# Kernel optimization log

Hardware: AMD Instinct MI355X
Metric: run time of the kernel (lower is better)

Reference implementation:

```python
import jax, jax.numpy as jnp
import numpy as np

UNITS = 1024
IN_DIM = 1024
BATCH = 64
SEQ = 512


def setup_inputs() -> dict:
    key = jax.random.key(0)
    k_x, k_wf, k_wb = jax.random.split(key, 3)
    x = jax.random.normal(k_x, (BATCH, SEQ, IN_DIM), dtype=jnp.float32)
    # keras 'random_normal' initializer -> stddev 0.05
    W_fwd = jax.random.normal(k_wf, (IN_DIM + UNITS, 4 * UNITS), dtype=jnp.float32) * 0.05
    b_fwd = jnp.zeros((4 * UNITS,), dtype=jnp.float32)
    W_bwd = jax.random.normal(k_wb, (IN_DIM + UNITS, 4 * UNITS), dtype=jnp.float32) * 0.05
    b_bwd = jnp.zeros((4 * UNITS,), dtype=jnp.float32)
    return {"x": x, "W_fwd": W_fwd, "b_fwd": b_fwd, "W_bwd": W_bwd, "b_bwd": b_bwd}


def _lstm_scan(x_tbd, W, b, units, reverse):
    # x_tbd: [T, B, D] time-major
    B = x_tbd.shape[1]
    h0 = jnp.zeros((B, units), dtype=x_tbd.dtype)
    c0 = jnp.zeros((B, units), dtype=x_tbd.dtype)

    def step(carry, x_t):
        h, c = carry
        z = jnp.concatenate([x_t, h], axis=-1) @ W + b  # [B, 4U]
        zi, zf, zo, zg = jnp.split(z, 4, axis=-1)
        c_new = jax.nn.sigmoid(zf) * c + jax.nn.sigmoid(zi) * jnp.tanh(zg)
        h_new = jax.nn.sigmoid(zo) * jnp.tanh(c_new)
        return (h_new, c_new), h_new

    _, hs = jax.lax.scan(step, (h0, c0), x_tbd, reverse=reverse)
    return hs  # [T, B, U], aligned with input time order


def reference(x, W_fwd, b_fwd, W_bwd, b_bwd):
    x_tbd = jnp.transpose(x, (1, 0, 2))  # [T, B, D]
    h_fwd = _lstm_scan(x_tbd, W_fwd, b_fwd, UNITS, reverse=False)
    h_bwd = _lstm_scan(x_tbd, W_bwd, b_bwd, UNITS, reverse=True)
    h = jnp.concatenate([h_fwd, h_bwd], axis=-1)  # [T, B, 2U]
    return jnp.transpose(h, (1, 0, 2))  # [B, T, 2U]
```

## Files before the change

kernel.cpp:

```cpp
#include <hip/hip_runtime.h>
#include <stdint.h>

#define B_ 64
#define T_ 512
#define D_ 1024
#define U_ 1024
#define G4_ 4096
#define M_ (B_ * T_)
#define ZLD 65

typedef unsigned short u16;
typedef float f32x4 __attribute__((ext_vector_type(4)));
typedef _Float16 f16x8 __attribute__((ext_vector_type(8)));
typedef unsigned short u16x4 __attribute__((ext_vector_type(4)));

__device__ __forceinline__ u16 f2h(float f) {
  union { _Float16 h; u16 u; } v; v.h = (_Float16)f; return v.u;
}
__device__ __forceinline__ float h2f(uint32_t u) {
  union { _Float16 h; u16 u; } v; v.u = (u16)u; return (float)v.h;
}
__device__ __forceinline__ float sigm(float x) { return 1.f / (1.f + __expf(-x)); }
__device__ __forceinline__ float tanhf_(float x) {
  x = fminf(12.f, fmaxf(-12.f, x));
  float e = __expf(2.f * x);
  return (e - 1.f) / (e + 1.f);
}

__device__ __forceinline__ void glds16(const void* g, void* l) {
  __builtin_amdgcn_global_load_lds(
      (const __attribute__((address_space(1))) uint32_t*)g,
      (__attribute__((address_space(3))) uint32_t*)l, 16, 0, 0);
}

template <int R>
__device__ __forceinline__ void stage_tile(const char* gbase, long gs, char* lds, int tid) {
  const int lane = tid & 63, wid = tid >> 6;
#pragma unroll
  for (int j = wid; j < R / 8; j += 4) {
    const int row = j * 8 + (lane >> 3);
    const int lg = ((lane & 7) * 16) ^ ((row & 7) << 4);
    glds16(gbase + (long)row * gs + lg, lds + j * 1024);
  }
}

__device__ __forceinline__ f16x8 read_frag(const char* lds, int row, int kbyte) {
  const int ph = row * 128 + (kbyte ^ ((row & 7) << 4));
  return *(const f16x8*)(lds + ph);
}

#define MFMA_(a, b, c) __builtin_amdgcn_mfma_f32_16x16x32_f16(a, b, c, 0, 0, 0)
#define BAR_LGKM() asm volatile("s_waitcnt lgkmcnt(0)\n\ts_barrier" ::: "memory")


__global__ __launch_bounds__(256) void cast_x_kernel(const float* __restrict__ x,
                                                     u16* __restrict__ xb) {
  const long n = (long)M_ * D_ / 4;
  for (long i = (long)blockIdx.x * blockDim.x + threadIdx.x; i < n;
       i += (long)gridDim.x * blockDim.x) {
    f32x4 v = ((const f32x4*)x)[i];
    u16x4 r;
#pragma unroll
    for (int j = 0; j < 4; ++j) r[j] = f2h(v[j]);
    ((u16x4*)xb)[i] = r;
  }
}

__global__ __launch_bounds__(256) void pack_wx_kernel(const float* __restrict__ Wf,
                                                      const float* __restrict__ Wb,
                                                      u16* __restrict__ wxT) {
  const int idx = blockIdx.x * 256 + threadIdx.x;
  const int p = idx & 4095;
  const int kc = (idx >> 12) & 63;
  const int d = (idx >> 18) & 1;
  const float* W = d ? Wb : Wf;
  const int orig = ((p >> 4) & 3) * 1024 + ((p >> 6) << 4) + (p & 15);
  u16* dst = wxT + ((long)d * G4_ + p) * 1024 + kc * 16;
  const float* src = W + (long)(kc * 16) * G4_ + orig;
#pragma unroll
  for (int j = 0; j < 16; ++j) dst[j] = f2h(src[(long)j * G4_]);
}

__global__ __launch_bounds__(256) void pack_whfl_kernel(const float* __restrict__ Wf,
                                                        const float* __restrict__ Wb,
                                                        u16* __restrict__ whfl) {
  const int idx = blockIdx.x * 256 + threadIdx.x;
  const int l = idx & 63;
  const int f = (idx >> 6) & 15;
  const int cc = (idx >> 10) & 7;
  const int ub = (idx >> 13) & 63;
  const int d = (idx >> 19) & 1;
  const float* W = d ? Wb : Wf;
  const int ni = f >> 2, kkl = f & 3;
  const int ocol = ni * 1024 + ub * 16 + (l & 15);
  const int krow = 1024 + cc * 128 + kkl * 32 + (l >> 4) * 8;
  u16* dst = whfl + ((((long)(d * 64 + ub) * 8 + cc) * 16 + f) << 9) + l * 8;
  const float* src = W + (long)krow * G4_ + ocol;
#pragma unroll
  for (int j = 0; j < 8; ++j) dst[j] = f2h(src[(long)j * G4_]);
}

__global__ __launch_bounds__(256) void gemm_xproj2(const u16* __restrict__ xbf,
                                                   const u16* __restrict__ wT,
                                                   const float* __restrict__ bF,
                                                   const float* __restrict__ bB,
                                                   u16* __restrict__ xp2) {
  __shared__ __align__(16) char smem[64 * 1024];
  const int tid = threadIdx.x, lane = tid & 63, wid = tid >> 6;
  const int wr = wid >> 1, wc = wid & 1;
  const int tm = blockIdx.x * 128, tn = blockIdx.y * 128, d = blockIdx.z;
  const char* Ag = (const char*)xbf + (long)tm * 2048;
  const char* Bg = (const char*)wT + ((long)d * G4_ + tn) * 2048;

  f32x4 acc[4][4];
#pragma unroll
  for (int mi = 0; mi < 4; ++mi)
#pragma unroll
    for (int ni = 0; ni < 4; ++ni)
#pragma unroll
      for (int v = 0; v < 4; ++v) acc[mi][ni][v] = 0.f;

  stage_tile<128>(Ag, 2048, smem, tid);
  stage_tile<128>(Bg, 2048, smem + 32768, tid);
  __syncthreads();
  const int rA = lane & 15, kb = (lane >> 4) * 16;

  for (int cc = 0; cc < 16; ++cc) {
    const int cur = cc & 1;
    char* Ac = smem + cur * 16384;
    char* Bc = smem + 32768 + cur * 16384;
    if (cc + 1 < 16) {
      stage_tile<128>(Ag + (cc + 1) * 128, 2048, smem + (cur ^ 1) * 16384, tid);
      stage_tile<128>(Bg + (cc + 1) * 128, 2048, smem + 32768 + (cur ^ 1) * 16384, tid);
    }
    f16x8 aF[4][2], bFr[4][2];
#pragma unroll
    for (int mi = 0; mi < 4; ++mi)
#pragma unroll
      for (int ks = 0; ks < 2; ++ks)
        aF[mi][ks] = read_frag(Ac, wr * 64 + mi * 16 + rA, kb + ks * 64);
#pragma unroll
    for (int ni = 0; ni < 4; ++ni)
#pragma unroll
      for (int ks = 0; ks < 2; ++ks)
        bFr[ni][ks] = read_frag(Bc, wc * 64 + ni * 16 + rA, kb + ks * 64);
#pragma unroll
    for (int mi = 0; mi < 4; ++mi)
#pragma unroll
      for (int ni = 0; ni < 4; ++ni)
#pragma unroll
        for (int ks = 0; ks < 2; ++ks)
          acc[mi][ni] = MFMA_(aF[mi][ks], bFr[ni][ks], acc[mi][ni]);
    __syncthreads();
  }

  const float* bias = d ? bB : bF;
#pragma unroll
  for (int ni = 0; ni < 4; ++ni) {
    const int p = tn + wc * 64 + ni * 16 + rA;
    const int orig = ((p >> 4) & 3) * 1024 + ((p >> 6) << 4) + (p & 15);
    const float bv = bias[orig];
    const int ub2 = p >> 6, pl = p & 63;
#pragma unroll
    for (int mi = 0; mi < 4; ++mi) {
      const int m0 = tm + wr * 64 + mi * 16 + (lane >> 4) * 4;
#pragma unroll
      for (int v = 0; v < 4; ++v) {
        const int m = m0 + v, b = m >> 9, t = m & 511;
        const int bh = b >> 5, br = b & 31;
        xp2[(((((long)d * T_ + t) * 64 + ub2) * 2 + bh) * 32 + br) * 64 + pl] =
            f2h(acc[mi][ni][v] + bv);
      }
    }
  }
}

__global__ __launch_bounds__(256) void lstm_step9(
    const u16* __restrict__ whfl, const u16* __restrict__ xp2,
    const u16* __restrict__ h_read, u16* __restrict__ h_write,
    float* __restrict__ cst, float* __restrict__ out, int s) {
  __shared__ __align__(16) char smem[131072 + ZLD * 32 * 4];
  float* zbuf = (float*)(smem + 131072);
  const int tid = threadIdx.x, lane = tid & 63, wid = tid >> 6;
  const int wm = wid & 1, kh = wid >> 1;
  const int g = blockIdx.x, ub = g >> 1, d = g & 1, bh = blockIdx.y;
  const int t = d ? (T_ - 1 - s) : s;
  const int rA = lane & 15, kq = lane >> 4;
  const char* wfl = (const char*)whfl + ((long)(d * 64 + ub) << 17);
  const char* xg = (const char*)xp2 + ((((long)d * T_ + t) * 64 + ub) * 2 + bh) * 4096;

  const int bl_g = tid >> 3, ui_g = (tid & 7) * 2;
  const int u_g = ub * 16 + ui_g;
  const int bglob = bh * 32 + bl_g;

  uint32_t xr[4];
  const char* xt = xg + (bl_g * 64 + ui_g) * 2;
#define XL(gg)                                                          \
  asm volatile("global_load_dword %0, %1, off offset:%2"               \
               : "=v"(xr[gg]) : "v"(xt), "n"(gg * 32) : "memory")
  XL(0); XL(1); XL(2); XL(3);
#undef XL
  const char* ah_base =
      (const char*)h_read +
      (((long)d * B_ + bh * 32 + wm * 16 + rA) * 1024 + kh * 512 + kq * 8) * 2;
  f16x8 ah[16];
#define AH(i)                                                           \
  asm volatile("global_load_dwordx4 %0, %1, off offset:%2"             \
               : "=v"(ah[i]) : "v"(ah_base), "n"(i * 64) : "memory")
  AH(0); AH(1); AH(2); AH(3); AH(4); AH(5); AH(6); AH(7);
  AH(8); AH(9); AH(10); AH(11); AH(12); AH(13); AH(14); AH(15);
#undef AH
#pragma unroll
  for (int q = 0; q < 32; ++q) {
    const int f = wid * 32 + q;
    glds16(wfl + (long)f * 1024 + lane * 16, smem + f * 1024);
  }
  const float2 creg = *(const float2*)(cst + ((long)d * B_ + bglob) * 1024 + u_g);

  asm volatile("s_waitcnt vmcnt(0)" ::: "memory");
  __builtin_amdgcn_sched_barrier(0);
  __builtin_amdgcn_s_barrier();
  asm volatile("" ::: "memory");

  f32x4 acc[4];
#pragma unroll
  for (int ni = 0; ni < 4; ++ni)
#pragma unroll
    for (int v = 0; v < 4; ++v) acc[ni][v] = 0.f;
  const char* bb = smem + (kh << 16) + (lane << 4);
#pragma unroll
  for (int kk = 0; kk < 16; ++kk) {
#pragma unroll
    for (int ni = 0; ni < 4; ++ni) {
      const f16x8 bF =
          *(const f16x8*)(bb + (((kk >> 2) * 16 + ni * 4 + (kk & 3)) << 10));
      acc[ni] = MFMA_(ah[kk], bF, acc[ni]);
    }
  }

  if (kh == 1) {
#pragma unroll
    for (int ni = 0; ni < 4; ++ni)
#pragma unroll
      for (int v = 0; v < 4; ++v)
        zbuf[(wm * 16 + kq * 4 + v) * ZLD + ni * 16 + rA] = acc[ni][v];
  }
  BAR_LGKM();
  if (kh == 0) {
#pragma unroll
    for (int ni = 0; ni < 4; ++ni)
#pragma unroll
      for (int v = 0; v < 4; ++v) {
        const int ix = (wm * 16 + kq * 4 + v) * ZLD + ni * 16 + rA;
        zbuf[ix] += acc[ni][v];
      }
  }
  BAR_LGKM();

  {
    const float* zb = zbuf + bl_g * ZLD + ui_g;
    const float zi0 = zb[0]  + h2f(xr[0] & 0xffff);
    const float zi1 = zb[1]  + h2f(xr[0] >> 16);
    const float zf0 = zb[16] + h2f(xr[1] & 0xffff);
    const float zf1 = zb[17] + h2f(xr[1] >> 16);
    const float zo0 = zb[32] + h2f(xr[2] & 0xffff);
    const float zo1 = zb[33] + h2f(xr[2] >> 16);
    const float zg0 = zb[48] + h2f(xr[3] & 0xffff);
    const float zg1 = zb[49] + h2f(xr[3] >> 16);
    const float cn0 = sigm(zf0) * creg.x + sigm(zi0) * tanhf_(zg0);
    const float cn1 = sigm(zf1) * creg.y + sigm(zi1) * tanhf_(zg1);
    const float hn0 = sigm(zo0) * tanhf_(cn0);
    const float hn1 = sigm(zo1) * tanhf_(cn1);

    float2 cw; cw.x = cn0; cw.y = cn1;
    *(float2*)(cst + ((long)d * B_ + bglob) * 1024 + u_g) = cw;
    const uint32_t hv = (uint32_t)f2h(hn0) | ((uint32_t)f2h(hn1) << 16);
    *(uint32_t*)(h_write + ((long)d * B_ + bglob) * 1024 + u_g) = hv;
    float2 o2; o2.x = hn0; o2.y = hn1;
    *(float2*)(out + ((long)bglob * T_ + t) * 2048 + d * 1024 + u_g) = o2;
  }
}


extern "C" void kernel_launch(void* const* d_in, const int* in_sizes, int n_in,
                              void* d_out, int out_size, void* d_ws, size_t ws_size,
                              hipStream_t stream) {
  const float* x = (const float*)d_in[0];
  const float* Wf = (const float*)d_in[1];
  const float* bfp = (const float*)d_in[2];
  const float* Wb = (const float*)d_in[3];
  const float* bbp = (const float*)d_in[4];
  float* out = (float*)d_out;
  char* ws = (char*)d_ws;

  size_t off = 0;
  auto alloc = [&](size_t bytes) {
    char* p = ws + off;
    off = (off + bytes + 255) & ~(size_t)255;
    return p;
  };
  u16* xbf = (u16*)alloc((size_t)M_ * D_ * 2);
  u16* wxT = (u16*)alloc((size_t)2 * G4_ * 1024 * 2);
  u16* whfl = (u16*)alloc((size_t)2 * 64 * 128 * 1024);
  u16* hst = (u16*)alloc((size_t)2 * 2 * B_ * U_ * 2);
  float* cst = (float*)alloc((size_t)2 * B_ * U_ * 4);
  u16* xproj = (u16*)alloc((size_t)2 * B_ * T_ * G4_ * 2);

  hipMemsetAsync(hst, 0, (size_t)2 * 2 * B_ * U_ * 2, stream);
  hipMemsetAsync(cst, 0, (size_t)2 * B_ * U_ * 4, stream);

  cast_x_kernel<<<2048, 256, 0, stream>>>(x, xbf);
  pack_wx_kernel<<<2048, 256, 0, stream>>>(Wf, Wb, wxT);
  pack_whfl_kernel<<<4096, 256, 0, stream>>>(Wf, Wb, whfl);

  dim3 gg(M_ / 128, G4_ / 128, 2);
  gemm_xproj2<<<gg, 256, 0, stream>>>(xbf, wxT, bfp, bbp, xproj);

  for (int s = 0; s < T_; ++s) {
    const u16* hr = hst + (size_t)(s & 1) * 2 * B_ * U_;
    u16* hw = hst + (size_t)((s + 1) & 1) * 2 * B_ * U_;
    lstm_step9<<<dim3(128, 2), 256, 0, stream>>>(whfl, xproj, hr, hw, cst, out, s);
  }
}
```

Baseline: 4.871 ms.

## Double-buffer recurrent weight staging and fuse gate epilogue into MFMA accumulators

```diff
diff --git a/kernel.cpp b/kernel.cpp
--- a/kernel.cpp
+++ b/kernel.cpp
@@ -50,7 +50,6 @@
 }
 
 #define MFMA_(a, b, c) __builtin_amdgcn_mfma_f32_16x16x32_f16(a, b, c, 0, 0, 0)
-#define BAR_LGKM() asm volatile("s_waitcnt lgkmcnt(0)\n\ts_barrier" ::: "memory")
 
 
 __global__ __launch_bounds__(256) void cast_x_kernel(const float* __restrict__ x,
@@ -175,12 +174,47 @@
   }
 }
 
-__global__ __launch_bounds__(256) void lstm_step9(
+
+__device__ __forceinline__ void stage_Wph(const char* wfl, int cc, char* slot, int tid) {
+  const int lane = tid & 63, wid = tid >> 6;
+#pragma unroll
+  for (int q = 0; q < 8; ++q) {
+    const int f = wid * 8 + q;
+    const int chunk = cc + (f >> 4) * 4;
+    glds16(wfl + (long)(chunk * 16 + (f & 15)) * 1024 + lane * 16,
+           slot + f * 1024);
+  }
+}
+
+template <int CC>
+__device__ __forceinline__ void kstep5(char* smem, const char* wfl, int tid,
+                                       int kh, const f16x8* ah, f32x4 (&acc)[4]) {
+  constexpr int N = (CC < 3) ? 8 : 0;
+  asm volatile("s_waitcnt vmcnt(%0)" :: "i"(N) : "memory");
+  __builtin_amdgcn_s_barrier();
+  asm volatile("" ::: "memory");
+  const char* Bslot = smem + (CC & 1) * 32768 + (kh << 14) + ((tid & 63) << 4);
+#pragma unroll
+  for (int kkl = 0; kkl < 4; ++kkl) {
+    const f16x8 a = ah[CC * 4 + kkl];
+#pragma unroll
+    for (int ni = 0; ni < 4; ++ni)
+      acc[ni] = MFMA_(a, *(const f16x8*)(Bslot + ((ni * 4 + kkl) << 10)), acc[ni]);
+  }
+  asm volatile("s_waitcnt lgkmcnt(0)" ::: "memory");
+  __builtin_amdgcn_sched_barrier(0);
+  __builtin_amdgcn_s_barrier();
+  asm volatile("" ::: "memory");
+  if (CC + 2 < 4)
+    stage_Wph(wfl, CC + 2, smem + (CC & 1) * 32768, tid);
+}
+
+__global__ __launch_bounds__(256) void lstm_step11(
     const u16* __restrict__ whfl, const u16* __restrict__ xp2,
     const u16* __restrict__ h_read, u16* __restrict__ h_write,
     float* __restrict__ cst, float* __restrict__ out, int s) {
-  __shared__ __align__(16) char smem[131072 + ZLD * 32 * 4];
-  float* zbuf = (float*)(smem + 131072);
+  __shared__ __align__(16) char smem[65536 + ZLD * 32 * 4];
+  float* zbuf = (float*)(smem + 65536);
   const int tid = threadIdx.x, lane = tid & 63, wid = tid >> 6;
   const int wm = wid & 1, kh = wid >> 1;
   const int g = blockIdx.x, ub = g >> 1, d = g & 1, bh = blockIdx.y;
@@ -188,96 +222,86 @@
   const int rA = lane & 15, kq = lane >> 4;
   const char* wfl = (const char*)whfl + ((long)(d * 64 + ub) << 17);
   const char* xg = (const char*)xp2 + ((((long)d * T_ + t) * 64 + ub) * 2 + bh) * 4096;
-
-  const int bl_g = tid >> 3, ui_g = (tid & 7) * 2;
-  const int u_g = ub * 16 + ui_g;
-  const int bglob = bh * 32 + bl_g;
-
-  uint32_t xr[4];
-  const char* xt = xg + (bl_g * 64 + ui_g) * 2;
-#define XL(gg)                                                          \
-  asm volatile("global_load_dword %0, %1, off offset:%2"               \
-               : "=v"(xr[gg]) : "v"(xt), "n"(gg * 32) : "memory")
-  XL(0); XL(1); XL(2); XL(3);
+  const int row0 = wm * 16 + kq * 4;
+
+  f32x4 creg;
+  uint32_t xr[4][4];
+  if (kh == 0) {
+    const float* cp = cst + ((((long)(d * 64 + ub) * 2 + bh) * 2 + wm) * 64 + lane) * 4;
+    asm volatile("global_load_dwordx4 %0, %1, off" : "=v"(creg) : "v"(cp) : "memory");
+#pragma unroll
+    for (int v = 0; v < 4; ++v) {
+      const char* xt = xg + ((row0 + v) * 64 + rA) * 2;
+#define XL(gg)                                                            \
+  asm volatile("global_load_ushort %0, %1, off offset:%2"                 \
+               : "=v"(xr[v][gg]) : "v"(xt), "n"(gg * 32) : "memory")
+      XL(0); XL(1); XL(2); XL(3);
 #undef XL
+    }
+  }
   const char* ah_base =
       (const char*)h_read +
       (((long)d * B_ + bh * 32 + wm * 16 + rA) * 1024 + kh * 512 + kq * 8) * 2;
   f16x8 ah[16];
-#define AH(i)                                                           \
-  asm volatile("global_load_dwordx4 %0, %1, off offset:%2"             \
+#define AH(i)                                                             \
+  asm volatile("global_load_dwordx4 %0, %1, off offset:%2"                \
                : "=v"(ah[i]) : "v"(ah_base), "n"(i * 64) : "memory")
   AH(0); AH(1); AH(2); AH(3); AH(4); AH(5); AH(6); AH(7);
   AH(8); AH(9); AH(10); AH(11); AH(12); AH(13); AH(14); AH(15);
 #undef AH
-#pragma unroll
-  for (int q = 0; q < 32; ++q) {
-    const int f = wid * 32 + q;
-    glds16(wfl + (long)f * 1024 + lane * 16, smem + f * 1024);
-  }
-  const float2 creg = *(const float2*)(cst + ((long)d * B_ + bglob) * 1024 + u_g);
-
-  asm volatile("s_waitcnt vmcnt(0)" ::: "memory");
-  __builtin_amdgcn_sched_barrier(0);
-  __builtin_amdgcn_s_barrier();
-  asm volatile("" ::: "memory");
+  stage_Wph(wfl, 0, smem, tid);
+  stage_Wph(wfl, 1, smem + 32768, tid);
 
   f32x4 acc[4];
 #pragma unroll
   for (int ni = 0; ni < 4; ++ni)
 #pragma unroll
     for (int v = 0; v < 4; ++v) acc[ni][v] = 0.f;
-  const char* bb = smem + (kh << 16) + (lane << 4);
-#pragma unroll
-  for (int kk = 0; kk < 16; ++kk) {
-#pragma unroll
-    for (int ni = 0; ni < 4; ++ni) {
-      const f16x8 bF =
-          *(const f16x8*)(bb + (((kk >> 2) * 16 + ni * 4 + (kk & 3)) << 10));
-      acc[ni] = MFMA_(ah[kk], bF, acc[ni]);
-    }
-  }
+
+  kstep5<0>(smem, wfl, tid, kh, ah, acc);
+  kstep5<1>(smem, wfl, tid, kh, ah, acc);
+  kstep5<2>(smem, wfl, tid, kh, ah, acc);
+  kstep5<3>(smem, wfl, tid, kh, ah, acc);
 
   if (kh == 1) {
 #pragma unroll
     for (int ni = 0; ni < 4; ++ni)
 #pragma unroll
       for (int v = 0; v < 4; ++v)
-        zbuf[(wm * 16 + kq * 4 + v) * ZLD + ni * 16 + rA] = acc[ni][v];
-  }
-  BAR_LGKM();
+        zbuf[(row0 + v) * ZLD + ni * 16 + rA] = acc[ni][v];
+  }
+  asm volatile("s_waitcnt lgkmcnt(0)\n\ts_barrier" ::: "memory");
+
   if (kh == 0) {
 #pragma unroll
     for (int ni = 0; ni < 4; ++ni)
 #pragma unroll
-      for (int v = 0; v < 4; ++v) {
-        const int ix = (wm * 16 + kq * 4 + v) * ZLD + ni * 16 + rA;
-        zbuf[ix] += acc[ni][v];
-      }
-  }
-  BAR_LGKM();
-
-  {
-    const float* zb = zbuf + bl_g * ZLD + ui_g;
-    const float zi0 = zb[0]  + h2f(xr[0] & 0xffff);
-    const float zi1 = zb[1]  + h2f(xr[0] >> 16);
-    const float zf0 = zb[16] + h2f(xr[1] & 0xffff);
-    const float zf1 = zb[17] + h2f(xr[1] >> 16);
-    const float zo0 = zb[32] + h2f(xr[2] & 0xffff);
-    const float zo1 = zb[33] + h2f(xr[2] >> 16);
-    const float zg0 = zb[48] + h2f(xr[3] & 0xffff);
-    const float zg1 = zb[49] + h2f(xr[3] >> 16);
-    const float cn0 = sigm(zf0) * creg.x + sigm(zi0) * tanhf_(zg0);
-    const float cn1 = sigm(zf1) * creg.y + sigm(zi1) * tanhf_(zg1);
-    const float hn0 = sigm(zo0) * tanhf_(cn0);
-    const float hn1 = sigm(zo1) * tanhf_(cn1);
-
-    float2 cw; cw.x = cn0; cw.y = cn1;
-    *(float2*)(cst + ((long)d * B_ + bglob) * 1024 + u_g) = cw;
-    const uint32_t hv = (uint32_t)f2h(hn0) | ((uint32_t)f2h(hn1) << 16);
-    *(uint32_t*)(h_write + ((long)d * B_ + bglob) * 1024 + u_g) = hv;
-    float2 o2; o2.x = hn0; o2.y = hn1;
-    *(float2*)(out + ((long)bglob * T_ + t) * 2048 + d * 1024 + u_g) = o2;
+      for (int v = 0; v < 4; ++v)
+        acc[ni][v] += zbuf[(row0 + v) * ZLD + ni * 16 + rA];
+
+    const int u_g = ub * 16 + rA;
+    float cnew[4], hn[4];
+#pragma unroll
+    for (int v = 0; v < 4; ++v) {
+      const float zi = acc[0][v] + h2f(xr[v][0]);
+      const float zf = acc[1][v] + h2f(xr[v][1]);
+      const float zo = acc[2][v] + h2f(xr[v][2]);
+      const float zg = acc[3][v] + h2f(xr[v][3]);
+      const float cn = sigm(zf) * creg[v] + sigm(zi) * tanhf_(zg);
+      cnew[v] = cn;
+      hn[v] = sigm(zo) * tanhf_(cn);
+    }
+    float* cp = cst + ((((long)(d * 64 + ub) * 2 + bh) * 2 + wm) * 64 + lane) * 4;
+    f32x4 cw;
+#pragma unroll
+    for (int v = 0; v < 4; ++v) cw[v] = cnew[v];
+    *(f32x4*)cp = cw;
+#pragma unroll
+    for (int v = 0; v < 4; ++v) {
+      const int brow = bh * 32 + row0 + v;
+      h_write[((long)d * B_ + brow) * 1024 + u_g] = f2h(hn[v]);
+      out[((long)brow * T_ + t) * 2048 + d * 1024 + u_g] = hn[v];
+    }
   }
 }
 
@@ -319,6 +343,6 @@
   for (int s = 0; s < T_; ++s) {
     const u16* hr = hst + (size_t)(s & 1) * 2 * B_ * U_;
     u16* hw = hst + (size_t)((s + 1) & 1) * 2 * B_ * U_;
-    lstm_step9<<<dim3(128, 2), 256, 0, stream>>>(whfl, xproj, hr, hw, cst, out, s);
-  }
-}
+    lstm_step11<<<dim3(128, 2), 256, 0, stream>>>(whfl, xproj, hr, hw, cst, out, s);
+  }
+}
```

Result: faster. 4.645 ms (-4.6%).
